# Performance work log

Hardware: AMD Instinct MI355X
Metric: run time of the kernel (lower is better)

Reference implementation:

```python
import jax, jax.numpy as jnp
import numpy as np

N_HEADS = 16


def setup_inputs() -> dict:
    key = jax.random.key(0)
    k1, k2, k3 = jax.random.split(key, 3)
    b, t, d = 2, 2048, 1024
    x = jax.random.normal(k1, (b, t, d), dtype=jnp.float32)
    # nn.Linear weights (stored here as [in, out]); 0.02 scale ~ standard init
    w_qkv = jax.random.normal(k2, (d, 3 * d), dtype=jnp.float32) * 0.02
    w_out = jax.random.normal(k3, (d, d), dtype=jnp.float32) * 0.02
    return {"x": x, "w_qkv": w_qkv, "w_out": w_out}


def reference(x, w_qkv, w_out):
    # Causal multi-head self-attention. The original module implements this
    # via a hand-rolled blockwise flash-attention loop with online softmax;
    # the intended math is exactly standard causal SDPA, expressed densely here.
    b, t, d = x.shape
    h = N_HEADS
    hd = d // h
    qkv = (x @ w_qkv).reshape(b, t, 3, h, hd)
    qkv = jnp.transpose(qkv, (2, 0, 3, 1, 4))  # [3, b, h, t, hd]
    q, k, v = qkv[0], qkv[1], qkv[2]
    scale = 1.0 / jnp.sqrt(jnp.float32(hd))
    s = jnp.einsum("bhqd,bhkd->bhqk", q, k) * scale  # [b, h, t, t]
    causal = jnp.tril(jnp.ones((t, t), dtype=bool))
    s = jnp.where(causal, s, -jnp.inf)
    p = jax.nn.softmax(s, axis=-1)
    o = jnp.einsum("bhqk,bhkd->bhqd", p, v)
    o = jnp.transpose(o, (0, 2, 1, 3)).reshape(b, t, d)
    return o @ w_out
```

## Files before the change

kernel.cpp:

```cpp
#include <hip/hip_runtime.h>

typedef float f32x4 __attribute__((ext_vector_type(4)));
typedef float f32x16 __attribute__((ext_vector_type(16)));
typedef short short8 __attribute__((ext_vector_type(8)));
typedef short short4_t __attribute__((ext_vector_type(4)));

#define GLOAD_LDS16(gp, lp) \
  __builtin_amdgcn_global_load_lds((const __attribute__((address_space(1))) void*)(gp), \
                                   (__attribute__((address_space(3))) void*)(lp), 16, 0, 0)

__device__ __forceinline__ short f2bf(float f){
  unsigned u = __builtin_bit_cast(unsigned, f);
  u += 0x7fffu + ((u >> 16) & 1u);
  return (short)(u >> 16);
}

__device__ __forceinline__ float exp2_fast(float x){
  return __builtin_amdgcn_exp2f(x);
}

__global__ __launch_bounds__(256) void prep_kernel(
    const float* __restrict__ x, const float* __restrict__ wqkv,
    const float* __restrict__ wout, short* __restrict__ xb,
    short* __restrict__ wqkvT, short* __restrict__ woutT)
{
  __shared__ float tile[32][33];
  const int bid = blockIdx.x, tid = threadIdx.x;
  if (bid < 512){
    int base = bid*2048 + tid;
    #pragma unroll
    for (int it=0; it<8; it++){
      int i = base + it*256;
      f32x4 v = ((const f32x4*)x)[i];
      short4_t s;
      s[0]=f2bf(v[0]); s[1]=f2bf(v[1]); s[2]=f2bf(v[2]); s[3]=f2bf(v[3]);
      ((short4_t*)xb)[i] = s;
    }
    return;
  }
  const float* w; short* wT; int N, idx;
  if (bid < 3584){ w = wqkv; wT = wqkvT; N = 3072; idx = bid - 512;  }
  else           { w = wout; wT = woutT; N = 1024; idx = bid - 3584; }
  const int K = 1024;
  int bn = (idx % (N >> 5)) * 32, bk = (idx / (N >> 5)) * 32;
  int tx = tid & 31, ty = tid >> 5;
  #pragma unroll
  for (int r=ty; r<32; r+=8) tile[r][tx] = w[(size_t)(bk+r)*N + bn + tx];
  __syncthreads();
  #pragma unroll
  for (int r=ty; r<32; r+=8) wT[(size_t)(bn+r)*K + bk + tx] = f2bf(tile[tx][r]);
}

template<int MODE>
__global__ __launch_bounds__(256) void gemm128_kernel(
    const short* __restrict__ A, const short* __restrict__ Bt,
    float* __restrict__ Cf, short* __restrict__ qb_, short* __restrict__ kb_,
    short* __restrict__ vb_, int M, int N, int K)
{
  __shared__ short a_lds[128*64];
  __shared__ short b_lds[128*64];
  const int tid = threadIdx.x;
  const int lane = tid & 63;
  const int l15 = lane & 15, lg = lane >> 4;
  const int w  = tid >> 6;
  const int wr = w >> 1, wc = w & 1;
  const int m0 = blockIdx.x * 128, n0 = blockIdx.y * 128;

  f32x4 acc[4][4];
  #pragma unroll
  for (int i=0;i<4;i++)
    #pragma unroll
    for (int j=0;j<4;j++) acc[i][j] = (f32x4){0.f,0.f,0.f,0.f};

  for (int kt = 0; kt < K; kt += 64){
    __syncthreads();
    #pragma unroll
    for (int i=0;i<4;i++){
      int u = i*256 + tid;
      int row = u >> 3, cu = u & 7;
      int kl = ((cu ^ (row & 7)) << 3);
      GLOAD_LDS16(A + (size_t)(m0+row)*K + kt + kl, a_lds + (size_t)(i*256 + (tid & ~63))*8);
    }
    #pragma unroll
    for (int i=0;i<4;i++){
      int u = i*256 + tid;
      int row = u >> 3, cu = u & 7;
      int kl = ((cu ^ (row & 7)) << 3);
      GLOAD_LDS16(Bt + (size_t)(n0+row)*K + kt + kl, b_lds + (size_t)(i*256 + (tid & ~63))*8);
    }
    asm volatile("s_waitcnt vmcnt(0)" ::: "memory");
    __syncthreads();

    #pragma unroll
    for (int kk=0;kk<2;kk++){
      short8 af[4], bfr[4];
      #pragma unroll
      for (int mi=0;mi<4;mi++){
        int row = wr*64 + mi*16 + l15;
        int uu = ((kk*4 + lg) ^ (row & 7));
        af[mi] = *(const short8*)&a_lds[row*64 + uu*8];
      }
      #pragma unroll
      for (int ni=0;ni<4;ni++){
        int row = wc*64 + ni*16 + l15;
        int uu = ((kk*4 + lg) ^ (row & 7));
        bfr[ni] = *(const short8*)&b_lds[row*64 + uu*8];
      }
      #pragma unroll
      for (int mi=0;mi<4;mi++)
        #pragma unroll
        for (int ni=0;ni<4;ni++)
          acc[mi][ni] = __builtin_amdgcn_mfma_f32_16x16x32_bf16(af[mi], bfr[ni], acc[mi][ni], 0,0,0);
    }
  }

  #pragma unroll
  for (int mi=0;mi<4;mi++){
    #pragma unroll
    for (int ni=0;ni<4;ni++){
      int col = n0 + wc*64 + ni*16 + l15;
      #pragma unroll
      for (int r=0;r<4;r++){
        int rowg = m0 + wr*64 + mi*16 + lg*4 + r;
        float v = acc[mi][ni][r];
        if (MODE == 0){
          Cf[(size_t)rowg*N + col] = v;
        } else {
          int three = col >> 10, hh = (col >> 6) & 15, e = col & 63;
          int bb = rowg >> 11, t = rowg & 2047;
          int bh = bb*16 + hh;
          if (three == 0)      qb_[((size_t)bh*2048 + t)*64 + e] = f2bf(v * (0.125f*1.44269504f));
          else if (three == 1) kb_[((size_t)bh*2048 + t)*64 + e] = f2bf(v);
          else                 vb_[((size_t)bh*2048 + t)*64 + e] = f2bf(v);
        }
      }
    }
  }
}

__global__ __launch_bounds__(256) void transpose_v_kernel(const short* __restrict__ vb,
                                                          short* __restrict__ vtb){
  __shared__ short tl[64][66];
  const int bh = blockIdx.x >> 5, t0 = (blockIdx.x & 31)*64;
  const int r = threadIdx.x >> 2, c4 = (threadIdx.x & 3)*16;
  const short* src = vb + ((size_t)bh*2048 + t0 + r)*64 + c4;
  short8 a0 = *(const short8*)(src);
  short8 a1 = *(const short8*)(src + 8);
  #pragma unroll
  for (int j=0;j<8;j++) tl[r][c4+j] = a0[j];
  #pragma unroll
  for (int j=0;j<8;j++) tl[r][c4+8+j] = a1[j];
  __syncthreads();
  short8 b0, b1;
  #pragma unroll
  for (int j=0;j<8;j++) b0[j] = tl[c4+j][r];
  #pragma unroll
  for (int j=0;j<8;j++) b1[j] = tl[c4+8+j][r];
  short* dst = vtb + ((size_t)bh*64 + r)*2048 + t0 + c4;
  *(short8*)dst = b0;
  *(short8*)(dst+8) = b1;
}

__global__ __launch_bounds__(256) void attn_kernel(
    const short* __restrict__ q, const short* __restrict__ kbuf,
    const short* __restrict__ vt, short* __restrict__ ob)
{
  __shared__ short k_lds[2][128*64];
  __shared__ short v_lds[2][64*128];

  const int tid = threadIdx.x, lane = tid & 63, w = tid >> 6;
  const int l31 = lane & 31, hi = lane >> 5;
  const int qi = blockIdx.x >> 5;
  const int qb = (qi < 8) ? (15 - qi) : (qi - 8);
  const int bh = blockIdx.x & 31;
  const int q0 = qb * 128;

  const short* qg = q + ((size_t)bh*2048 + q0 + w*32 + l31)*64 + hi*8;
  short8 qf[4];
  #pragma unroll
  for (int kk=0;kk<4;kk++) qf[kk] = *(const short8*)(qg + kk*16);

  f32x16 o_acc[2];
  #pragma unroll
  for (int oc=0;oc<2;oc++)
    #pragma unroll
    for (int r=0;r<16;r++) o_acc[oc][r] = 0.f;
  float mreg = -1e30f, lreg = 0.f;

  const int sw = l31 & 7;
  int kro[4], vro[8];
  #pragma unroll
  for (int kk=0;kk<4;kk++) kro[kk] = l31*128 + (((kk*2+hi)^sw) << 4);
  #pragma unroll
  for (int ks=0;ks<8;ks++) vro[ks] = l31*256 + (((ks*2+hi)^sw) << 4);

  const int xk = ((tid & 7) ^ ((tid >> 3) & 7)) * 8;
  const int xv = ((tid & 15) ^ ((tid >> 4) & 7)) * 8;
  const short* kp = kbuf + (size_t)bh*2048*64 + (size_t)(tid >> 3)*64 + xk;
  const short* vp = vt   + (size_t)bh*64*2048 + (size_t)(tid >> 4)*2048 + xv;
  const int dst = (tid & ~63)*8;

  const int n = qb + 1;
  #pragma unroll
  for (int i=0;i<4;i++) GLOAD_LDS16(kp + i*2048,  &k_lds[0][i*2048 + dst]);
  #pragma unroll
  for (int i=0;i<4;i++) GLOAD_LDS16(vp + i*32768, &v_lds[0][i*2048 + dst]);
  kp += 8192; vp += 128;

  for (int s = 0; s < n; s++){
    const int cur = s & 1;
    if (s + 1 < n){
      #pragma unroll
      for (int i=0;i<4;i++) GLOAD_LDS16(kp + i*2048,  &k_lds[cur^1][i*2048 + dst]);
      #pragma unroll
      for (int i=0;i<4;i++) GLOAD_LDS16(vp + i*32768, &v_lds[cur^1][i*2048 + dst]);
      kp += 8192; vp += 128;
      asm volatile("s_waitcnt vmcnt(8)" ::: "memory");
    } else {
      asm volatile("s_waitcnt vmcnt(0)" ::: "memory");
    }
    __builtin_amdgcn_s_barrier();

    const char* kl_ = (const char*)&k_lds[cur][0];
    const char* vl_ = (const char*)&v_lds[cur][0];

    f32x16 sacc[4];
    #pragma unroll
    for (int ct=0;ct<4;ct++)
      #pragma unroll
      for (int r=0;r<16;r++) sacc[ct][r] = 0.f;
    __builtin_amdgcn_s_setprio(1);
    #pragma unroll
    for (int kk=0;kk<4;kk++){
      #pragma unroll
      for (int ct=0;ct<4;ct++){
        short8 kf = *(const short8*)(kl_ + kro[kk] + ct*4096);
        sacc[ct] = __builtin_amdgcn_mfma_f32_32x32x16_bf16(kf, qf[kk], sacc[ct], 0,0,0);
      }
    }
    __builtin_amdgcn_s_setprio(0);

    if (s == qb){
      const int qloc = w*32 + l31 - 4*hi;
      #pragma unroll
      for (int ct=0;ct<4;ct++)
        #pragma unroll
        for (int r=0;r<16;r++)
          if (ct*32 + (r&3) + 8*(r>>2) > qloc) sacc[ct][r] = -1e30f;
    }

    float pmax = sacc[0][0];
    #pragma unroll
    for (int ct=0;ct<4;ct++)
      #pragma unroll
      for (int r=0;r<16;r++) pmax = fmaxf(pmax, sacc[ct][r]);
    pmax = fmaxf(pmax, __shfl_xor(pmax, 32));

    if (!__all(pmax - mreg <= 8.0f)){
      float mnew = fmaxf(mreg, pmax);
      float alpha = exp2_fast(mreg - mnew);
      mreg = mnew;
      lreg *= alpha;
      float aRow[16];
      #pragma unroll
      for (int r=0;r<16;r++) aRow[r] = __shfl(alpha, (r&3) + 8*(r>>2) + 4*hi);
      #pragma unroll
      for (int oc=0;oc<2;oc++)
        #pragma unroll
        for (int r=0;r<16;r++) o_acc[oc][r] *= aRow[r];
    }

    float sum = 0.f;
    #pragma unroll
    for (int ct=0;ct<4;ct++){
      float pv[16];
      #pragma unroll
      for (int r=0;r<16;r++){ pv[r] = exp2_fast(sacc[ct][r] - mreg); sum += pv[r]; }
      unsigned pk[8];
      #pragma unroll
      for (int t=0;t<8;t++)
        asm("v_cvt_pk_bf16_f32 %0, %1, %2" : "=v"(pk[t]) : "v"(pv[2*t]), "v"(pv[2*t+1]));
      #pragma unroll
      for (int kss=0;kss<2;kss++){
        const int W = 4*kss;
        unsigned x0 = pk[W],   x2 = pk[W+2];
        unsigned x1 = pk[W+1], x3 = pk[W+3];
        asm("v_permlane32_swap_b32 %0, %1" : "+v"(x0), "+v"(x2));
        asm("v_permlane32_swap_b32 %0, %1" : "+v"(x1), "+v"(x3));
        uint4 pau = {x0, x1, x2, x3};
        short8 pa = __builtin_bit_cast(short8, pau);
        __builtin_amdgcn_s_setprio(1);
        #pragma unroll
        for (int oc=0;oc<2;oc++){
          short8 vf = *(const short8*)(vl_ + vro[2*ct+kss] + oc*8192);
          o_acc[oc] = __builtin_amdgcn_mfma_f32_32x32x16_bf16(pa, vf, o_acc[oc], 0,0,0);
        }
        __builtin_amdgcn_s_setprio(0);
      }
    }
    sum += __shfl_xor(sum, 32);
    lreg += sum;

    __builtin_amdgcn_s_barrier();
  }

  const int bb = bh >> 4, hh = bh & 15;
  #pragma unroll
  for (int r=0;r<16;r++){
    float lf = __shfl(lreg, (r&3) + 8*(r>>2) + 4*hi);
    float inv = 1.0f / lf;
    int t = q0 + w*32 + (r&3) + 8*(r>>2) + 4*hi;
    size_t base = ((size_t)(bb*2048 + t))*1024 + (size_t)hh*64 + l31;
    ob[base]      = f2bf(o_acc[0][r] * inv);
    ob[base + 32] = f2bf(o_acc[1][r] * inv);
  }
}

extern "C" void kernel_launch(void* const* d_in, const int* in_sizes, int n_in,
                              void* d_out, int out_size, void* d_ws, size_t ws_size,
                              hipStream_t stream) {
  const float* x     = (const float*)d_in[0];
  const float* w_qkv = (const float*)d_in[1];
  const float* w_out = (const float*)d_in[2];
  float* out = (float*)d_out;

  char* ws = (char*)d_ws;
  short* xb    = (short*)(ws);
  short* wqkvT = (short*)(ws + (8u  << 20));
  short* woutT = (short*)(ws + (14u << 20));
  short* qbuf  = (short*)(ws + (16u << 20));
  short* kbuf  = (short*)(ws + (24u << 20));
  short* vbuf  = (short*)(ws + (32u << 20));
  short* vtbuf = (short*)(ws + (40u << 20));
  short* obuf  = vbuf;

  prep_kernel<<<4608, 256, 0, stream>>>(x, w_qkv, w_out, xb, wqkvT, woutT);
  gemm128_kernel<1><<<dim3(32,24), 256, 0, stream>>>(xb, wqkvT, nullptr,
                                                     qbuf, kbuf, vbuf, 4096, 3072, 1024);
  transpose_v_kernel<<<1024, 256, 0, stream>>>(vbuf, vtbuf);
  attn_kernel<<<dim3(512), 256, 0, stream>>>(qbuf, kbuf, vtbuf, obuf);
  gemm128_kernel<0><<<dim3(32,8), 256, 0, stream>>>(obuf, woutT, out,
                                                    nullptr, nullptr, nullptr, 4096, 1024, 1024);
}
```

Baseline: 115.4 us.

## Use 256x256 pipelined 8-wave GEMM for QKV projection

Replaces the 128x128 single-buffered QKV projection GEMM with a 256x256 tile, 512-thread kernel. It uses an 8-slot LDS ring of 32-wide K chunks, prefetches the next chunks while MFMAs run, and adds explicit barriers, waitcnts and setprio to interleave loads with compute. The aim is to hide global-load latency and raise operand reuse per block. The cost is only 192 blocks, which may underfill the 256 CUs, plus higher register and LDS pressure. The output projection keeps the old 128 kernel, now a non-template version.

```diff
diff --git a/kernel.cpp b/kernel.cpp
--- a/kernel.cpp
+++ b/kernel.cpp
@@ -52,77 +52,140 @@
 }
 
 template<int MODE>
-__global__ __launch_bounds__(256) void gemm128_kernel(
+__global__ __launch_bounds__(512) void gemm256_kernel(
     const short* __restrict__ A, const short* __restrict__ Bt,
     float* __restrict__ Cf, short* __restrict__ qb_, short* __restrict__ kb_,
     short* __restrict__ vb_, int M, int N, int K)
 {
-  __shared__ short a_lds[128*64];
-  __shared__ short b_lds[128*64];
-  const int tid = threadIdx.x;
-  const int lane = tid & 63;
-  const int l15 = lane & 15, lg = lane >> 4;
+  __shared__ short lds[8*8192];
+  const int tid = threadIdx.x, lane = tid & 63;
+  const int l15 = lane & 15, lg = (lane >> 4) & 3;
   const int w  = tid >> 6;
-  const int wr = w >> 1, wc = w & 1;
-  const int m0 = blockIdx.x * 128, n0 = blockIdx.y * 128;
-
-  f32x4 acc[4][4];
-  #pragma unroll
-  for (int i=0;i<4;i++)
-    #pragma unroll
-    for (int j=0;j<4;j++) acc[i][j] = (f32x4){0.f,0.f,0.f,0.f};
-
-  for (int kt = 0; kt < K; kt += 64){
-    __syncthreads();
-    #pragma unroll
-    for (int i=0;i<4;i++){
-      int u = i*256 + tid;
-      int row = u >> 3, cu = u & 7;
-      int kl = ((cu ^ (row & 7)) << 3);
-      GLOAD_LDS16(A + (size_t)(m0+row)*K + kt + kl, a_lds + (size_t)(i*256 + (tid & ~63))*8);
-    }
-    #pragma unroll
-    for (int i=0;i<4;i++){
-      int u = i*256 + tid;
-      int row = u >> 3, cu = u & 7;
-      int kl = ((cu ^ (row & 7)) << 3);
-      GLOAD_LDS16(Bt + (size_t)(n0+row)*K + kt + kl, b_lds + (size_t)(i*256 + (tid & ~63))*8);
-    }
-    asm volatile("s_waitcnt vmcnt(0)" ::: "memory");
-    __syncthreads();
-
-    #pragma unroll
-    for (int kk=0;kk<2;kk++){
-      short8 af[4], bfr[4];
-      #pragma unroll
-      for (int mi=0;mi<4;mi++){
-        int row = wr*64 + mi*16 + l15;
-        int uu = ((kk*4 + lg) ^ (row & 7));
-        af[mi] = *(const short8*)&a_lds[row*64 + uu*8];
-      }
-      #pragma unroll
-      for (int ni=0;ni<4;ni++){
-        int row = wc*64 + ni*16 + l15;
-        int uu = ((kk*4 + lg) ^ (row & 7));
-        bfr[ni] = *(const short8*)&b_lds[row*64 + uu*8];
-      }
-      #pragma unroll
-      for (int mi=0;mi<4;mi++)
-        #pragma unroll
-        for (int ni=0;ni<4;ni++)
-          acc[mi][ni] = __builtin_amdgcn_mfma_f32_16x16x32_bf16(af[mi], bfr[ni], acc[mi][ni], 0,0,0);
-    }
-  }
-
-  #pragma unroll
-  for (int mi=0;mi<4;mi++){
-    #pragma unroll
-    for (int ni=0;ni<4;ni++){
-      int col = n0 + wc*64 + ni*16 + l15;
+  const int wm = w >> 2, wn = w & 3;
+  const int m0 = blockIdx.x * 256, n0 = blockIdx.y * 256;
+
+  const int r0 = tid >> 2, r1 = 128 + r0;
+  const int c0 = tid & 3;
+  const int u0 = c0 ^ ((r0 ^ (r0 >> 2)) & 3);
+  const int u1 = c0 ^ ((r1 ^ (r1 >> 2)) & 3);
+  const short* pA0 = A  + (size_t)(m0 + r0)*K + u0*8;
+  const short* pA1 = A  + (size_t)(m0 + r1)*K + u1*8;
+  const short* pB0 = Bt + (size_t)(n0 + r0)*K + u0*8;
+  const short* pB1 = Bt + (size_t)(n0 + r1)*K + u1*8;
+  const int d0 = (tid & ~63)*8;
+  const int d1 = (512 + (tid & ~63))*8;
+
+  const int su = (l15 ^ (l15 >> 2)) & 3;
+  const int abase = (wm*128 + l15)*64 + ((lg ^ su) << 4);
+  const int bbase = (wn*64  + l15)*64 + ((lg ^ su) << 4);
+
+  f32x4 acc[8][4];
+  #pragma unroll
+  for (int m=0;m<8;m++)
+    #pragma unroll
+    for (int n=0;n<4;n++) acc[m][n] = (f32x4){0.f,0.f,0.f,0.f};
+
+  auto stage = [&](const short* p0, const short* p1, int kcol, int slot){
+    GLOAD_LDS16(p0 + kcol, &lds[slot*8192 + d0]);
+    GLOAD_LDS16(p1 + kcol, &lds[slot*8192 + d1]);
+  };
+
+  const int NT = K >> 6;
+  stage(pA0, pA1, 0,  0);
+  stage(pB0, pB1, 0,  1);
+  stage(pA0, pA1, 32, 2);
+  stage(pB0, pB1, 32, 3);
+  asm volatile("s_waitcnt vmcnt(4)" ::: "memory");
+  __builtin_amdgcn_s_barrier();
+
+  for (int t = 0; t < NT; ++t){
+    const int b = (t*4) & 7;
+    const char* LA0 = (const char*)lds + (size_t)b*16384;
+    const char* LB0 = (const char*)lds + (size_t)((b+1)&7)*16384;
+    const char* LA1 = (const char*)lds + (size_t)((b+2)&7)*16384;
+    const char* LB1 = (const char*)lds + (size_t)((b+3)&7)*16384;
+    const int nk = (t+1)*64;
+    const bool pf = (t+1 < NT);
+    short8 af[8], bf[4];
+
+    #pragma unroll
+    for (int m=0;m<8;m++) af[m] = *(const short8*)(LA0 + abase + m*1024);
+    bf[0] = *(const short8*)(LB0 + bbase);
+    bf[1] = *(const short8*)(LB0 + bbase + 1024);
+    if (pf) stage(pA0, pA1, nk, (b+4)&7);
+    __builtin_amdgcn_s_barrier();
+    asm volatile("s_waitcnt lgkmcnt(0)" ::: "memory");
+    __builtin_amdgcn_sched_barrier(0);
+    __builtin_amdgcn_s_setprio(1);
+    #pragma unroll
+    for (int m=0;m<8;m++){
+      acc[m][0] = __builtin_amdgcn_mfma_f32_16x16x32_bf16(af[m], bf[0], acc[m][0], 0,0,0);
+      acc[m][1] = __builtin_amdgcn_mfma_f32_16x16x32_bf16(af[m], bf[1], acc[m][1], 0,0,0);
+    }
+    __builtin_amdgcn_s_setprio(0);
+    __builtin_amdgcn_s_barrier();
+
+    bf[2] = *(const short8*)(LB0 + bbase + 2048);
+    bf[3] = *(const short8*)(LB0 + bbase + 3072);
+    if (pf){ stage(pB0, pB1, nk, (b+5)&7);
+             asm volatile("s_waitcnt vmcnt(4)" ::: "memory"); }
+    else   { asm volatile("s_waitcnt vmcnt(0)" ::: "memory"); }
+    __builtin_amdgcn_s_barrier();
+    asm volatile("s_waitcnt lgkmcnt(0)" ::: "memory");
+    __builtin_amdgcn_sched_barrier(0);
+    __builtin_amdgcn_s_setprio(1);
+    #pragma unroll
+    for (int m=0;m<8;m++){
+      acc[m][2] = __builtin_amdgcn_mfma_f32_16x16x32_bf16(af[m], bf[2], acc[m][2], 0,0,0);
+      acc[m][3] = __builtin_amdgcn_mfma_f32_16x16x32_bf16(af[m], bf[3], acc[m][3], 0,0,0);
+    }
+    __builtin_amdgcn_s_setprio(0);
+    __builtin_amdgcn_s_barrier();
+
+    #pragma unroll
+    for (int m=0;m<8;m++) af[m] = *(const short8*)(LA1 + abase + m*1024);
+    bf[0] = *(const short8*)(LB1 + bbase);
+    bf[1] = *(const short8*)(LB1 + bbase + 1024);
+    if (pf) stage(pA0, pA1, nk + 32, (b+6)&7);
+    __builtin_amdgcn_s_barrier();
+    asm volatile("s_waitcnt lgkmcnt(0)" ::: "memory");
+    __builtin_amdgcn_sched_barrier(0);
+    __builtin_amdgcn_s_setprio(1);
+    #pragma unroll
+    for (int m=0;m<8;m++){
+      acc[m][0] = __builtin_amdgcn_mfma_f32_16x16x32_bf16(af[m], bf[0], acc[m][0], 0,0,0);
+      acc[m][1] = __builtin_amdgcn_mfma_f32_16x16x32_bf16(af[m], bf[1], acc[m][1], 0,0,0);
+    }
+    __builtin_amdgcn_s_setprio(0);
+    __builtin_amdgcn_s_barrier();
+
+    bf[2] = *(const short8*)(LB1 + bbase + 2048);
+    bf[3] = *(const short8*)(LB1 + bbase + 3072);
+    if (pf){ stage(pB0, pB1, nk + 32, (b+7)&7);
+             asm volatile("s_waitcnt vmcnt(4)" ::: "memory"); }
+    else   { asm volatile("s_waitcnt vmcnt(0)" ::: "memory"); }
+    __builtin_amdgcn_s_barrier();
+    asm volatile("s_waitcnt lgkmcnt(0)" ::: "memory");
+    __builtin_amdgcn_sched_barrier(0);
+    __builtin_amdgcn_s_setprio(1);
+    #pragma unroll
+    for (int m=0;m<8;m++){
+      acc[m][2] = __builtin_amdgcn_mfma_f32_16x16x32_bf16(af[m], bf[2], acc[m][2], 0,0,0);
+      acc[m][3] = __builtin_amdgcn_mfma_f32_16x16x32_bf16(af[m], bf[3], acc[m][3], 0,0,0);
+    }
+    __builtin_amdgcn_s_setprio(0);
+    __builtin_amdgcn_s_barrier();
+  }
+
+  #pragma unroll
+  for (int m=0;m<8;m++){
+    #pragma unroll
+    for (int n=0;n<4;n++){
+      int col = n0 + wn*64 + n*16 + l15;
       #pragma unroll
       for (int r=0;r<4;r++){
-        int rowg = m0 + wr*64 + mi*16 + lg*4 + r;
-        float v = acc[mi][ni][r];
+        int rowg = m0 + wm*128 + m*16 + lg*4 + r;
+        float v = acc[m][n][r];
         if (MODE == 0){
           Cf[(size_t)rowg*N + col] = v;
         } else {
@@ -133,6 +196,81 @@
           else if (three == 1) kb_[((size_t)bh*2048 + t)*64 + e] = f2bf(v);
           else                 vb_[((size_t)bh*2048 + t)*64 + e] = f2bf(v);
         }
+      }
+    }
+  }
+}
+
+__global__ __launch_bounds__(256) void gemm128_kernel(
+    const short* __restrict__ A, const short* __restrict__ Bt,
+    float* __restrict__ Cf, int M, int N, int K)
+{
+  __shared__ short a_lds[128*64];
+  __shared__ short b_lds[128*64];
+  const int tid = threadIdx.x;
+  const int lane = tid & 63;
+  const int l15 = lane & 15, lg = lane >> 4;
+  const int w  = tid >> 6;
+  const int wr = w >> 1, wc = w & 1;
+  const int m0 = blockIdx.x * 128, n0 = blockIdx.y * 128;
+
+  f32x4 acc[4][4];
+  #pragma unroll
+  for (int i=0;i<4;i++)
+    #pragma unroll
+    for (int j=0;j<4;j++) acc[i][j] = (f32x4){0.f,0.f,0.f,0.f};
+
+  for (int kt = 0; kt < K; kt += 64){
+    __syncthreads();
+    #pragma unroll
+    for (int i=0;i<4;i++){
+      int u = i*256 + tid;
+      int row = u >> 3, cu = u & 7;
+      int kl = ((cu ^ (row & 7)) << 3);
+      GLOAD_LDS16(A + (size_t)(m0+row)*K + kt + kl, a_lds + (size_t)(i*256 + (tid & ~63))*8);
+    }
+    #pragma unroll
+    for (int i=0;i<4;i++){
+      int u = i*256 + tid;
+      int row = u >> 3, cu = u & 7;
+      int kl = ((cu ^ (row & 7)) << 3);
+      GLOAD_LDS16(Bt + (size_t)(n0+row)*K + kt + kl, b_lds + (size_t)(i*256 + (tid & ~63))*8);
+    }
+    asm volatile("s_waitcnt vmcnt(0)" ::: "memory");
+    __syncthreads();
+
+    #pragma unroll
+    for (int kk=0;kk<2;kk++){
+      short8 af[4], bfr[4];
+      #pragma unroll
+      for (int mi=0;mi<4;mi++){
+        int row = wr*64 + mi*16 + l15;
+        int uu = ((kk*4 + lg) ^ (row & 7));
+        af[mi] = *(const short8*)&a_lds[row*64 + uu*8];
+      }
+      #pragma unroll
+      for (int ni=0;ni<4;ni++){
+        int row = wc*64 + ni*16 + l15;
+        int uu = ((kk*4 + lg) ^ (row & 7));
+        bfr[ni] = *(const short8*)&b_lds[row*64 + uu*8];
+      }
+      #pragma unroll
+      for (int mi=0;mi<4;mi++)
+        #pragma unroll
+        for (int ni=0;ni<4;ni++)
+          acc[mi][ni] = __builtin_amdgcn_mfma_f32_16x16x32_bf16(af[mi], bfr[ni], acc[mi][ni], 0,0,0);
+    }
+  }
+
+  #pragma unroll
+  for (int mi=0;mi<4;mi++){
+    #pragma unroll
+    for (int ni=0;ni<4;ni++){
+      int col = n0 + wc*64 + ni*16 + l15;
+      #pragma unroll
+      for (int r=0;r<4;r++){
+        int rowg = m0 + wr*64 + mi*16 + lg*4 + r;
+        Cf[(size_t)rowg*N + col] = acc[mi][ni][r];
       }
     }
   }
@@ -335,10 +473,9 @@
   short* obuf  = vbuf;
 
   prep_kernel<<<4608, 256, 0, stream>>>(x, w_qkv, w_out, xb, wqkvT, woutT);
-  gemm128_kernel<1><<<dim3(32,24), 256, 0, stream>>>(xb, wqkvT, nullptr,
+  gemm256_kernel<1><<<dim3(16,12), 512, 0, stream>>>(xb, wqkvT, nullptr,
                                                      qbuf, kbuf, vbuf, 4096, 3072, 1024);
   transpose_v_kernel<<<1024, 256, 0, stream>>>(vbuf, vtbuf);
   attn_kernel<<<dim3(512), 256, 0, stream>>>(qbuf, kbuf, vtbuf, obuf);
-  gemm128_kernel<0><<<dim3(32,8), 256, 0, stream>>>(obuf, woutT, out,
-                                                    nullptr, nullptr, nullptr, 4096, 1024, 1024);
-}
+  gemm128_kernel<<<dim3(32,8), 256, 0, stream>>>(obuf, woutT, out, 4096, 1024, 1024);
+}
```

New measurement: 122.5 us. 6.2% more time.
